# Optimization experiments

Hardware: AMD Instinct MI355X
Metric: run time of the kernel (lower is better)

## Reference

```python
import jax, jax.numpy as jnp
import numpy as np

D_MODEL = 1024
ADAPTER_DIM = 64
NUM_EXPERTS = 4


def setup_inputs() -> dict:
    key = jax.random.key(0)
    kx, kd, ku, kg, kb = jax.random.split(key, 5)
    x = jax.random.normal(kx, (4, 4096, D_MODEL), dtype=jnp.float32)
    # Per-expert LoRA weights, stored contraction-ready:
    # W_down[e]: d_model -> adapter  (shape [E, d, a])
    # W_up[e]:   adapter -> d_model  (shape [E, a, d])
    s_down = 1.0 / np.sqrt(D_MODEL)
    s_up = 1.0 / np.sqrt(ADAPTER_DIM)
    W_down = jax.random.uniform(kd, (NUM_EXPERTS, D_MODEL, ADAPTER_DIM), jnp.float32, -s_down, s_down)
    W_up = jax.random.uniform(ku, (NUM_EXPERTS, ADAPTER_DIM, D_MODEL), jnp.float32, -s_up, s_up)
    W_gate = jax.random.uniform(kg, (D_MODEL, NUM_EXPERTS), jnp.float32, -s_down, s_down)
    b_gate = jax.random.uniform(kb, (NUM_EXPERTS,), jnp.float32, -s_down, s_down)
    return {"x": x, "W_down": W_down, "W_up": W_up, "W_gate": W_gate, "b_gate": b_gate}


def reference(x, W_down, W_up, W_gate, b_gate):
    # gate_weights: [b, s, e]
    gate_weights = jax.nn.softmax(jnp.einsum("bsd,de->bse", x, W_gate) + b_gate, axis=-1)
    # down: [b, s, e, a]
    down = jnp.einsum("bsd,eda->bsea", x, W_down)
    # gated weighted sum of expert up-projections, fused: [b, s, d]
    out = jnp.einsum("bsea,ead,bse->bsd", down, W_up, gate_weights)
    return out
```

## Files before the change

### kernel.cpp

```cpp
#include <hip/hip_runtime.h>

typedef __attribute__((ext_vector_type(8))) short bf16x8;
typedef __attribute__((ext_vector_type(4))) float f32x4;
typedef unsigned short u16;

#define D_MODEL 1024
#define ROWS 32

#define WD_FRAGS (17 * 32)
#define WU_FRAGS (64 * 8)
#define WD_ELEMS (WD_FRAGS * 512)
#define WU_ELEMS (WU_FRAGS * 512)

#define LDS_TOTAL 49664
#define TB_STRIDE 260

__device__ __forceinline__ u16 f2bf(float f) {
  union { float f; unsigned u; } v; v.f = f;
  return (u16)((v.u + 0x7fffu + ((v.u >> 16) & 1u)) >> 16);
}

__global__ void lora_prep(const float* __restrict__ Wd, const float* __restrict__ Wu,
                          const float* __restrict__ Wg,
                          u16* __restrict__ wd_pack, u16* __restrict__ wu_pack) {
  int idx = blockIdx.x * 256 + threadIdx.x;
  if (idx < WD_ELEMS) {
    int frag = idx >> 9, w = idx & 511;
    int lane = w >> 3, j = w & 7;
    int nt = frag >> 5, kt = frag & 31;
    int k = kt * 32 + (lane >> 4) * 8 + j;
    int col = nt * 16 + (lane & 15);
    float v;
    if (col < 256) {
      v = Wd[((col >> 6) * 1024 + k) * 64 + (col & 63)];
    } else {
      int c2 = col - 256;
      v = (c2 < 4) ? Wg[k * 4 + c2] : 0.f;
    }
    wd_pack[idx] = f2bf(v);
  } else if (idx < WD_ELEMS + WU_ELEMS) {
    int u = idx - WD_ELEMS;
    int frag = u >> 9, w = u & 511;
    int lane = w >> 3, j = w & 7;
    int nt = frag >> 3, kt = frag & 7;
    int k = kt * 32 + (lane >> 4) * 8 + j;
    int col = nt * 16 + (lane & 15);
    wu_pack[u] = f2bf(Wu[((k >> 6) * 64 + (k & 63)) * 1024 + col]);
  }
}

__device__ __forceinline__ void pack_store(char* dst, int r, int col, float4 v0, float4 v1) {
  bf16x8 h;
  h[0] = (short)f2bf(v0.x); h[1] = (short)f2bf(v0.y);
  h[2] = (short)f2bf(v0.z); h[3] = (short)f2bf(v0.w);
  h[4] = (short)f2bf(v1.x); h[5] = (short)f2bf(v1.y);
  h[6] = (short)f2bf(v1.z); h[7] = (short)f2bf(v1.w);
  int cb = col * 2;
  *(bf16x8*)(dst + r * 512 + (cb ^ ((r & 7) << 4))) = h;
}

__global__ __launch_bounds__(512, 4) void lora_main(
    const float* __restrict__ x, const float* __restrict__ b_gate,
    const u16* __restrict__ wd_pack, const u16* __restrict__ wu_pack,
    float* __restrict__ out) {
  extern __shared__ char smem[];
  float* g = (float*)(smem + 32768);

  const int tid = threadIdx.x;
  const int lane = tid & 63;
  const int wave = tid >> 6;
  const int l15 = lane & 15;
  const int lg = lane >> 4;
  const size_t row0 = (size_t)blockIdx.x * ROWS;
  const float* xblk = x + row0 * D_MODEL;

  f32x4 acc[2][2];
  f32x4 accg[2];
#pragma unroll
  for (int i = 0; i < 2; ++i)
#pragma unroll
    for (int r = 0; r < 2; ++r) acc[i][r] = {0.f, 0.f, 0.f, 0.f};
#pragma unroll
  for (int r = 0; r < 2; ++r) accg[r] = {0.f, 0.f, 0.f, 0.f};

#pragma unroll
  for (int it = 0; it < 2; ++it) {
    int flat = it * 4096 + tid * 8;
    int r = flat >> 8, col = flat & 255;
    float4 v0 = *(const float4*)(xblk + r * D_MODEL + col);
    float4 v1 = *(const float4*)(xblk + r * D_MODEL + col + 4);
    pack_store(smem, r, col, v0, v1);
  }
  __syncthreads();

  float4 pre[4];
  bf16x8 bq[3][2];
  bf16x8 gq[3];
#pragma unroll 1
  for (int c = 0; c < 4; ++c) {
    if (c < 3) {
      const float* src = xblk + (c + 1) * 256;
#pragma unroll
      for (int it = 0; it < 2; ++it) {
        int flat = it * 4096 + tid * 8;
        int r = flat >> 8, col = flat & 255;
        pre[2 * it]     = *(const float4*)(src + r * D_MODEL + col);
        pre[2 * it + 1] = *(const float4*)(src + r * D_MODEL + col + 4);
      }
    }
    const char* buf = smem + (c & 1) * 16384;
#pragma unroll
    for (int pk = 0; pk < 2; ++pk) {
      int ktg = c * 8 + pk;
#pragma unroll
      for (int i = 0; i < 2; ++i)
        bq[pk][i] = *(const bf16x8*)(wd_pack + (size_t)((wave + i * 8) * 32 + ktg) * 512 + lane * 8);
      if (wave == 7)
        gq[pk] = *(const bf16x8*)(wd_pack + (size_t)(512 + ktg) * 512 + lane * 8);
    }
#pragma unroll
    for (int ks = 0; ks < 8; ++ks) {
      const int s = ks % 3;
      if (ks < 6) {
        int ktg2 = c * 8 + ks + 2;
        int s2 = (ks + 2) % 3;
#pragma unroll
        for (int i = 0; i < 2; ++i)
          bq[s2][i] = *(const bf16x8*)(wd_pack + (size_t)((wave + i * 8) * 32 + ktg2) * 512 + lane * 8);
        if (wave == 7)
          gq[s2] = *(const bf16x8*)(wd_pack + (size_t)(512 + ktg2) * 512 + lane * 8);
      }
      bf16x8 a[2];
#pragma unroll
      for (int r = 0; r < 2; ++r) {
        int rr = r * 16 + l15;
        int cb = (ks * 32 + lg * 8) * 2;
        a[r] = *(const bf16x8*)(buf + rr * 512 + (cb ^ ((rr & 7) << 4)));
      }
#pragma unroll
      for (int i = 0; i < 2; ++i)
#pragma unroll
        for (int r = 0; r < 2; ++r)
          acc[i][r] = __builtin_amdgcn_mfma_f32_16x16x32_bf16(a[r], bq[s][i], acc[i][r], 0, 0, 0);
      if (wave == 7) {
#pragma unroll
        for (int r = 0; r < 2; ++r)
          accg[r] = __builtin_amdgcn_mfma_f32_16x16x32_bf16(a[r], gq[s], accg[r], 0, 0, 0);
      }
    }
    if (c < 3) {
      char* dst = smem + ((c + 1) & 1) * 16384;
#pragma unroll
      for (int it = 0; it < 2; ++it) {
        int flat = it * 4096 + tid * 8;
        int r = flat >> 8, col = flat & 255;
        pack_store(dst, r, col, pre[2 * it], pre[2 * it + 1]);
      }
    }
    __syncthreads();
  }

  if (wave == 7 && l15 < 4) {
#pragma unroll
    for (int r = 0; r < 2; ++r)
#pragma unroll
      for (int j = 0; j < 4; ++j)
        g[(r * 16 + lg * 4 + j) * 4 + l15] = accg[r][j];
  }
  __syncthreads();
  if (tid < ROWS) {
    float v0 = g[tid * 4 + 0] + b_gate[0];
    float v1 = g[tid * 4 + 1] + b_gate[1];
    float v2 = g[tid * 4 + 2] + b_gate[2];
    float v3 = g[tid * 4 + 3] + b_gate[3];
    float m = fmaxf(fmaxf(v0, v1), fmaxf(v2, v3));
    float e0 = expf(v0 - m), e1 = expf(v1 - m), e2 = expf(v2 - m), e3 = expf(v3 - m);
    float inv = 1.f / (e0 + e1 + e2 + e3);
    g[tid * 4 + 0] = e0 * inv; g[tid * 4 + 1] = e1 * inv;
    g[tid * 4 + 2] = e2 * inv; g[tid * 4 + 3] = e3 * inv;
  }
  __syncthreads();

  char* ds = smem;
#pragma unroll
  for (int i = 0; i < 2; ++i) {
    int nt = wave + i * 8;
    int col = nt * 16 + l15;
    int e = nt >> 2;
    int cb = col * 2;
#pragma unroll
    for (int r = 0; r < 2; ++r) {
#pragma unroll
      for (int j = 0; j < 4; ++j) {
        int row = r * 16 + lg * 4 + j;
        float val = acc[i][r][j] * g[row * 4 + e];
        *(u16*)(ds + row * 512 + (cb ^ ((row & 7) << 4))) = f2bf(val);
      }
    }
  }
  __syncthreads();

  float* tb = (float*)(smem + 16384);
  bf16x8 b2[3][2];
#pragma unroll 1
  for (int nc = 0; nc < 4; ++nc) {
    f32x4 acc2[2][2];
#pragma unroll
    for (int i = 0; i < 2; ++i)
#pragma unroll
      for (int r = 0; r < 2; ++r) acc2[i][r] = {0.f, 0.f, 0.f, 0.f};
#pragma unroll
    for (int pk = 0; pk < 2; ++pk)
#pragma unroll
      for (int i = 0; i < 2; ++i)
        b2[pk][i] = *(const bf16x8*)(wu_pack + (size_t)((nc * 16 + wave * 2 + i) * 8 + pk) * 512 + lane * 8);
#pragma unroll
    for (int ks = 0; ks < 8; ++ks) {
      const int s = ks % 3;
      if (ks < 6) {
        int s2 = (ks + 2) % 3;
#pragma unroll
        for (int i = 0; i < 2; ++i)
          b2[s2][i] = *(const bf16x8*)(wu_pack + (size_t)((nc * 16 + wave * 2 + i) * 8 + ks + 2) * 512 + lane * 8);
      }
      bf16x8 a[2];
#pragma unroll
      for (int r = 0; r < 2; ++r) {
        int rr = r * 16 + l15;
        int cb = (ks * 32 + lg * 8) * 2;
        a[r] = *(const bf16x8*)(ds + rr * 512 + (cb ^ ((rr & 7) << 4)));
      }
#pragma unroll
      for (int i = 0; i < 2; ++i)
#pragma unroll
        for (int r = 0; r < 2; ++r)
          acc2[i][r] = __builtin_amdgcn_mfma_f32_16x16x32_bf16(a[r], b2[s][i], acc2[i][r], 0, 0, 0);
    }
#pragma unroll
    for (int i = 0; i < 2; ++i) {
      int cl = wave * 32 + i * 16 + l15;
#pragma unroll
      for (int r = 0; r < 2; ++r)
#pragma unroll
        for (int j = 0; j < 4; ++j)
          tb[(r * 16 + lg * 4 + j) * TB_STRIDE + cl] = acc2[i][r][j];
    }
    __syncthreads();
#pragma unroll
    for (int it = 0; it < 4; ++it) {
      int flat = it * 2048 + tid * 4;
      int row = flat >> 8, col = flat & 255;
      float4 v = *(const float4*)(tb + row * TB_STRIDE + col);
      *(float4*)(out + (row0 + row) * D_MODEL + nc * 256 + col) = v;
    }
    __syncthreads();
  }
}

extern "C" void kernel_launch(void* const* d_in, const int* in_sizes, int n_in,
                              void* d_out, int out_size, void* d_ws, size_t ws_size,
                              hipStream_t stream) {
  const float* x  = (const float*)d_in[0];
  const float* Wd = (const float*)d_in[1];
  const float* Wu = (const float*)d_in[2];
  const float* Wg = (const float*)d_in[3];
  const float* bg = (const float*)d_in[4];
  float* out = (float*)d_out;
  const int M = in_sizes[0] / D_MODEL;

  u16* wd_pack = (u16*)d_ws;
  u16* wu_pack = wd_pack + WD_ELEMS;

  const int total = WD_ELEMS + WU_ELEMS;
  lora_prep<<<(total + 255) / 256, 256, 0, stream>>>(Wd, Wu, Wg, wd_pack, wu_pack);
  lora_main<<<M / ROWS, 512, LDS_TOTAL, stream>>>(x, bg, wd_pack, wu_pack, out);
}
```

Baseline: 51.33 us.

## Compute gate softmax redundantly per wave with shuffles, dropping LDS barriers

Every wave now loads the gate weight fragments and runs the gate MFMAs itself, so the softmax can be done in registers. Cross-lane shuffles over the four expert columns replace the LDS round-trip and the single-thread softmax, which removes three block-wide barriers. The barrier after the last down-projection chunk is also dropped, and s_setprio raises wave priority around the MFMA bursts. The trade-off is extra gate MFMAs and weight loads in all eight waves instead of one.

```diff
diff --git a/kernel.cpp b/kernel.cpp
--- a/kernel.cpp
+++ b/kernel.cpp
@@ -64,7 +64,6 @@
     const u16* __restrict__ wd_pack, const u16* __restrict__ wu_pack,
     float* __restrict__ out) {
   extern __shared__ char smem[];
-  float* g = (float*)(smem + 32768);
 
   const int tid = threadIdx.x;
   const int lane = tid & 63;
@@ -115,8 +114,7 @@
 #pragma unroll
       for (int i = 0; i < 2; ++i)
         bq[pk][i] = *(const bf16x8*)(wd_pack + (size_t)((wave + i * 8) * 32 + ktg) * 512 + lane * 8);
-      if (wave == 7)
-        gq[pk] = *(const bf16x8*)(wd_pack + (size_t)(512 + ktg) * 512 + lane * 8);
+      gq[pk] = *(const bf16x8*)(wd_pack + (size_t)(512 + ktg) * 512 + lane * 8);
     }
 #pragma unroll
     for (int ks = 0; ks < 8; ++ks) {
@@ -127,8 +125,7 @@
 #pragma unroll
         for (int i = 0; i < 2; ++i)
           bq[s2][i] = *(const bf16x8*)(wd_pack + (size_t)((wave + i * 8) * 32 + ktg2) * 512 + lane * 8);
-        if (wave == 7)
-          gq[s2] = *(const bf16x8*)(wd_pack + (size_t)(512 + ktg2) * 512 + lane * 8);
+        gq[s2] = *(const bf16x8*)(wd_pack + (size_t)(512 + ktg2) * 512 + lane * 8);
       }
       bf16x8 a[2];
 #pragma unroll
@@ -137,16 +134,16 @@
         int cb = (ks * 32 + lg * 8) * 2;
         a[r] = *(const bf16x8*)(buf + rr * 512 + (cb ^ ((rr & 7) << 4)));
       }
+      __builtin_amdgcn_s_setprio(1);
 #pragma unroll
       for (int i = 0; i < 2; ++i)
 #pragma unroll
         for (int r = 0; r < 2; ++r)
           acc[i][r] = __builtin_amdgcn_mfma_f32_16x16x32_bf16(a[r], bq[s][i], acc[i][r], 0, 0, 0);
-      if (wave == 7) {
-#pragma unroll
-        for (int r = 0; r < 2; ++r)
-          accg[r] = __builtin_amdgcn_mfma_f32_16x16x32_bf16(a[r], gq[s], accg[r], 0, 0, 0);
-      }
+#pragma unroll
+      for (int r = 0; r < 2; ++r)
+        accg[r] = __builtin_amdgcn_mfma_f32_16x16x32_bf16(a[r], gq[s], accg[r], 0, 0, 0);
+      __builtin_amdgcn_s_setprio(0);
     }
     if (c < 3) {
       char* dst = smem + ((c + 1) & 1) * 16384;
@@ -156,30 +153,26 @@
         int r = flat >> 8, col = flat & 255;
         pack_store(dst, r, col, pre[2 * it], pre[2 * it + 1]);
       }
-    }
-    __syncthreads();
-  }
-
-  if (wave == 7 && l15 < 4) {
+      __syncthreads();
+    }
+  }
+
+  float gown[2][4];
+  {
+    const float bg = b_gate[l15 & 3];
 #pragma unroll
     for (int r = 0; r < 2; ++r)
 #pragma unroll
-      for (int j = 0; j < 4; ++j)
-        g[(r * 16 + lg * 4 + j) * 4 + l15] = accg[r][j];
-  }
-  __syncthreads();
-  if (tid < ROWS) {
-    float v0 = g[tid * 4 + 0] + b_gate[0];
-    float v1 = g[tid * 4 + 1] + b_gate[1];
-    float v2 = g[tid * 4 + 2] + b_gate[2];
-    float v3 = g[tid * 4 + 3] + b_gate[3];
-    float m = fmaxf(fmaxf(v0, v1), fmaxf(v2, v3));
-    float e0 = expf(v0 - m), e1 = expf(v1 - m), e2 = expf(v2 - m), e3 = expf(v3 - m);
-    float inv = 1.f / (e0 + e1 + e2 + e3);
-    g[tid * 4 + 0] = e0 * inv; g[tid * 4 + 1] = e1 * inv;
-    g[tid * 4 + 2] = e2 * inv; g[tid * 4 + 3] = e3 * inv;
-  }
-  __syncthreads();
+      for (int j = 0; j < 4; ++j) {
+        float v = accg[r][j] + bg;
+        float m1 = fmaxf(v, __shfl_xor(v, 1));
+        float mx = fmaxf(m1, __shfl_xor(m1, 2));
+        float ex = expf(v - mx);
+        float s1 = ex + __shfl_xor(ex, 1);
+        float sm = s1 + __shfl_xor(s1, 2);
+        gown[r][j] = ex / sm;
+      }
+  }
 
   char* ds = smem;
 #pragma unroll
@@ -187,13 +180,15 @@
     int nt = wave + i * 8;
     int col = nt * 16 + l15;
     int e = nt >> 2;
+    int src = lg * 16 + e;
     int cb = col * 2;
 #pragma unroll
     for (int r = 0; r < 2; ++r) {
 #pragma unroll
       for (int j = 0; j < 4; ++j) {
+        float gv = __shfl(gown[r][j], src);
         int row = r * 16 + lg * 4 + j;
-        float val = acc[i][r][j] * g[row * 4 + e];
+        float val = acc[i][r][j] * gv;
         *(u16*)(ds + row * 512 + (cb ^ ((row & 7) << 4))) = f2bf(val);
       }
     }
@@ -230,11 +225,13 @@
         int cb = (ks * 32 + lg * 8) * 2;
         a[r] = *(const bf16x8*)(ds + rr * 512 + (cb ^ ((rr & 7) << 4)));
       }
+      __builtin_amdgcn_s_setprio(1);
 #pragma unroll
       for (int i = 0; i < 2; ++i)
 #pragma unroll
         for (int r = 0; r < 2; ++r)
           acc2[i][r] = __builtin_amdgcn_mfma_f32_16x16x32_bf16(a[r], b2[s][i], acc2[i][r], 0, 0, 0);
+      __builtin_amdgcn_s_setprio(0);
     }
 #pragma unroll
     for (int i = 0; i < 2; ++i) {
```

After: 53.72 us. 1.05x slower.
